# Kernel optimization log

Hardware: AMD Instinct MI355X
Metric: run time of the kernel (lower is better)

The kernel has to match this reference:

```python
import jax, jax.numpy as jnp
import numpy as np

B = 128
H = 512
S_TOK = 512
S_DESC = 128
N_NODES = 65536
MARGIN = 0.05
COS_EPS = 1e-8


def setup_inputs() -> dict:
    key = jax.random.key(0)
    ks = jax.random.split(key, 26)
    sc = 1.0 / np.sqrt(H)
    inp = {
        "token_feat": jax.random.normal(ks[0], (B, S_TOK, H), jnp.float32),
        "token_len": jnp.maximum(jax.random.randint(ks[1], (B,), 0, S_TOK), 1),
        "node_h": jax.random.normal(ks[2], (N_NODES, H), jnp.float32),
        "seg_ids": jnp.sort(jax.random.randint(ks[3], (N_NODES,), 0, B)),
        "desc_anchor_feat": jax.random.normal(ks[4], (B, S_DESC, H), jnp.float32),
        "desc_anchor_len": jnp.maximum(jax.random.randint(ks[5], (B,), 0, S_DESC), 1),
        "desc_neg_feat": jax.random.normal(ks[6], (B, S_DESC, H), jnp.float32),
        "desc_neg_len": jnp.maximum(jax.random.randint(ks[7], (B,), 0, S_DESC), 1),
        # attention params: Linear(H,H) weight/bias, Linear(H,1) weight/bias
        "Wt": jax.random.normal(ks[8], (H, H), jnp.float32) * sc,
        "bt": jax.random.normal(ks[9], (H,), jnp.float32) * sc,
        "vt": jax.random.normal(ks[10], (H,), jnp.float32) * sc,
        "ct": jax.random.normal(ks[11], (), jnp.float32) * sc,
        "Wa": jax.random.normal(ks[12], (H, H), jnp.float32) * sc,
        "ba": jax.random.normal(ks[13], (H,), jnp.float32) * sc,
        "va": jax.random.normal(ks[14], (H,), jnp.float32) * sc,
        "ca": jax.random.normal(ks[15], (), jnp.float32) * sc,
        "Wd": jax.random.normal(ks[16], (H, H), jnp.float32) * sc,
        "bd": jax.random.normal(ks[17], (H,), jnp.float32) * sc,
        "vd": jax.random.normal(ks[18], (H,), jnp.float32) * sc,
        "cd": jax.random.normal(ks[19], (), jnp.float32) * sc,
        "Wf": jax.random.normal(ks[20], (2 * H, H), jnp.float32) * sc,
        "bf": jax.random.normal(ks[21], (H,), jnp.float32) * sc,
    }
    return inp


def masked_attn_pool(feat, lens, W, b, v, c):
    # feat: [B,S,H]; lens: [B]. Masked softmax attention pooling == the
    # per-sample masked_select + softmax + bmm loop, vectorized.
    logits = jnp.einsum("bsh,h->bs", jnp.tanh(jnp.einsum("bsh,hk->bsk", feat, W) + b), v) + c
    mask = jnp.arange(feat.shape[1])[None, :] < lens[:, None]
    logits = jnp.where(mask, logits, -jnp.inf)
    w = jax.nn.softmax(logits, axis=1)  # [B,S]
    return jnp.einsum("bs,bsh->bh", w, feat)


def segment_attn_pool(h, seg, W, b, v, c, num_segments):
    # h: [N,H] packed node states; seg: [N] sample id. Per-segment softmax attn
    # pooling == the per-sample slice + softmax + bmm loop over tree_node_num.
    logits = jnp.tanh(h @ W + b) @ v + c  # [N]
    m = jax.ops.segment_max(logits, seg, num_segments=num_segments)
    e = jnp.exp(logits - m[seg])
    denom = jax.ops.segment_sum(e, seg, num_segments=num_segments)
    w = e / denom[seg]
    return jax.ops.segment_sum(w[:, None] * h, seg, num_segments=num_segments)


def cosine_sim(a, b):
    na = jnp.maximum(jnp.linalg.norm(a, axis=1), COS_EPS)
    nb = jnp.maximum(jnp.linalg.norm(b, axis=1), COS_EPS)
    return jnp.sum(a * b, axis=1) / (na * nb)


def reference(token_feat, token_len, node_h, seg_ids, desc_anchor_feat,
              desc_anchor_len, desc_neg_feat, desc_neg_len,
              Wt, bt, vt, ct, Wa, ba, va, ca, Wd, bd, vd, cd, Wf, bf):
    # token modality (use_token_attn, then use_tanh)
    tok = jnp.tanh(masked_attn_pool(token_feat, token_len, Wt, bt, vt, ct))
    # AST modality: use_tanh applies to node states BEFORE attention
    hn = jnp.tanh(node_h)
    ast = jnp.tanh(segment_attn_pool(hn, seg_ids, Wa, ba, va, ca, B))
    code_feat = jnp.tanh(jnp.concatenate([tok, ast], axis=1) @ Wf + bf)
    # desc modality: attn pool, use_tanh, then the extra unconditional tanh
    da = jnp.tanh(jnp.tanh(masked_attn_pool(desc_anchor_feat, desc_anchor_len, Wd, bd, vd, cd)))
    dn = jnp.tanh(jnp.tanh(masked_attn_pool(desc_neg_feat, desc_neg_len, Wd, bd, vd, cd)))
    anchor_sim = cosine_sim(code_feat, da)
    neg_sim = cosine_sim(code_feat, dn)
    loss = jnp.mean(jnp.maximum(MARGIN - anchor_sim + neg_sim, 1e-6))
    return loss
```

## Files before the change

kernel.cpp:

```cpp
#include <hip/hip_runtime.h>
#include <math.h>

#define HDIM 512
#define BATCH 128

typedef _Float16 f16x8 __attribute__((ext_vector_type(8)));
typedef float f32x4 __attribute__((ext_vector_type(4)));

__device__ __forceinline__ float fast_tanh(float x) {
  float e = __expf(2.0f * x);
  return 1.0f - 2.0f / (e + 1.0f);
}

__device__ __forceinline__ void gload_lds16(const void* g, void* l) {
  __builtin_amdgcn_global_load_lds(
      (const __attribute__((address_space(1))) unsigned int*)g,
      (__attribute__((address_space(3))) unsigned int*)l, 16, 0, 0);
}

template <bool TANH>
__global__ __launch_bounds__(256) void cvt_tile_kernel(
    const float* __restrict__ A, _Float16* __restrict__ A2,
    int Mtot, int m_off, int Mrows) {
  const int total = Mrows * 64;
  for (int i = blockIdx.x * 256 + threadIdx.x; i < total; i += gridDim.x * 256) {
    const int m = i >> 6, c = i & 63;
    const int kt = c >> 3, cc = c & 7;
    const float* src = A + (size_t)m * HDIM + c * 8;
    const float4 x = ((const float4*)src)[0];
    const float4 y = ((const float4*)src)[1];
    f16x8 h;
    if (TANH) {
      h[0] = (_Float16)fast_tanh(x.x); h[1] = (_Float16)fast_tanh(x.y);
      h[2] = (_Float16)fast_tanh(x.z); h[3] = (_Float16)fast_tanh(x.w);
      h[4] = (_Float16)fast_tanh(y.x); h[5] = (_Float16)fast_tanh(y.y);
      h[6] = (_Float16)fast_tanh(y.z); h[7] = (_Float16)fast_tanh(y.w);
    } else {
      h[0] = (_Float16)x.x; h[1] = (_Float16)x.y;
      h[2] = (_Float16)x.z; h[3] = (_Float16)x.w;
      h[4] = (_Float16)y.x; h[5] = (_Float16)y.y;
      h[6] = (_Float16)y.z; h[7] = (_Float16)y.w;
    }
    const int dr = m_off + m;
    char* dst = (char*)A2 + ((size_t)kt * Mtot + dr) * 128 + ((cc * 16) ^ ((dr & 7) << 4));
    *(f16x8*)dst = h;
  }
}

__global__ __launch_bounds__(256) void cvt_w3_kernel(
    const float* __restrict__ Wt, const float* __restrict__ Wa,
    const float* __restrict__ Wd, _Float16* __restrict__ W2t,
    _Float16* __restrict__ W2a, _Float16* __restrict__ W2d) {
  const int i = blockIdx.x * 256 + threadIdx.x;
  if (i >= 512 * 64) return;
  const float* W = (blockIdx.y == 0) ? Wt : (blockIdx.y == 1) ? Wa : Wd;
  _Float16* W2 = (blockIdx.y == 0) ? W2t : (blockIdx.y == 1) ? W2a : W2d;
  const int n = i & 511, g = i >> 9;
  const int kt = g >> 3, cc = g & 7;
  f16x8 h;
#pragma unroll
  for (int j = 0; j < 8; ++j)
    h[j] = (_Float16)W[(size_t)(kt * 64 + cc * 8 + j) * HDIM + n];
  char* dst = (char*)W2 + ((size_t)kt * 512 + n) * 128 + ((cc * 16) ^ ((n & 7) << 4));
  *(f16x8*)dst = h;
}

__global__ __launch_bounds__(512) void gemm_logits_pipe_kernel(
    const _Float16* __restrict__ A2, const _Float16* __restrict__ W2,
    const float* __restrict__ bias, const float* __restrict__ vvec,
    float* __restrict__ logits, int M) {
  __shared__ __align__(16) _Float16 As[2][128 * 64];
  __shared__ __align__(16) _Float16 Bs[2][128 * 64];

  const int tid = threadIdx.x;
  const int nwg = gridDim.x;
  const int qq = nwg >> 3;
  const int raw = blockIdx.x;
  const int swz = (raw & 7) * qq + (raw >> 3);
  const int nb = swz & 3;
  const int mb = swz >> 2;
  const size_t m0 = (size_t)mb * 128;
  const int n0 = nb * 128;

  const int lane = tid & 63, wid = tid >> 6;
  const int tx = lane & 15, qd = lane >> 4;
  const int wm = wid >> 1;
  const int wn = wid & 1;

  const char* gA = (const char*)A2 + m0 * 128;
  const char* gB = (const char*)W2 + (size_t)n0 * 128;
  const size_t sA = (size_t)M * 128;
  const size_t sB = (size_t)512 * 128;
  const int lo = tid * 16;
  const int wlo = wid * 1024;

  f32x4 acc[2][4];
#pragma unroll
  for (int i = 0; i < 2; ++i)
#pragma unroll
    for (int j = 0; j < 4; ++j) acc[i][j] = (f32x4){0.f, 0.f, 0.f, 0.f};

  auto STAGE = [&](int buf, int kt) {
    const char* a = gA + (size_t)kt * sA;
    const char* b = gB + (size_t)kt * sB;
#pragma unroll
    for (int p = 0; p < 2; ++p) {
      gload_lds16(a + lo + p * 8192, (char*)As[buf] + wlo + p * 8192);
      gload_lds16(b + lo + p * 8192, (char*)Bs[buf] + wlo + p * 8192);
    }
  };

  auto COMPUTE = [&](int buf) {
#pragma unroll
    for (int ks = 0; ks < 2; ++ks) {
      f16x8 aF[2], bF[4];
#pragma unroll
      for (int f = 0; f < 2; ++f) {
        const int row = wm * 32 + f * 16 + tx;
        int by = row * 128 + (ks * 32 + qd * 8) * 2;
        by ^= (row & 7) << 4;
        aF[f] = *(const f16x8*)((const char*)As[buf] + by);
      }
#pragma unroll
      for (int f = 0; f < 4; ++f) {
        const int n = wn * 64 + f * 16 + tx;
        int by = n * 128 + (ks * 32 + qd * 8) * 2;
        by ^= (n & 7) << 4;
        bF[f] = *(const f16x8*)((const char*)Bs[buf] + by);
      }
#pragma unroll
      for (int i = 0; i < 2; ++i)
#pragma unroll
        for (int j = 0; j < 4; ++j)
          acc[i][j] = __builtin_amdgcn_mfma_f32_16x16x32_f16(aF[i], bF[j], acc[i][j], 0, 0, 0);
    }
  };

  STAGE(0, 0);
#pragma unroll
  for (int t = 0; t < 8; ++t) {
    const int cur = t & 1;
    if (t < 7) {
      STAGE(cur ^ 1, t + 1);
      asm volatile("s_waitcnt vmcnt(4)" ::: "memory");
    } else {
      asm volatile("s_waitcnt vmcnt(0)" ::: "memory");
    }
    asm volatile("" ::: "memory");
    __builtin_amdgcn_s_barrier();
    asm volatile("" ::: "memory");
    __builtin_amdgcn_s_setprio(1);
    COMPUTE(cur);
    __builtin_amdgcn_s_setprio(0);
    asm volatile("" ::: "memory");
    __builtin_amdgcn_s_barrier();
    asm volatile("" ::: "memory");
  }

  float vv[4], bb[4];
#pragma unroll
  for (int j = 0; j < 4; ++j) {
    const int n = n0 + wn * 64 + j * 16 + tx;
    vv[j] = vvec[n];
    bb[j] = bias[n];
  }
#pragma unroll
  for (int i = 0; i < 2; ++i) {
#pragma unroll
    for (int r = 0; r < 4; ++r) {
      float s = 0.0f;
#pragma unroll
      for (int j = 0; j < 4; ++j)
        s = fmaf(vv[j], fast_tanh(acc[i][j][r] + bb[j]), s);
      s += __shfl_xor(s, 1);
      s += __shfl_xor(s, 2);
      s += __shfl_xor(s, 4);
      s += __shfl_xor(s, 8);
      if (tx == 0)
        atomicAdd(&logits[m0 + wm * 32 + i * 16 + qd * 4 + r], s);
    }
  }
}


__global__ void zero_kernel(float* __restrict__ p, int n) {
  const int i = blockIdx.x * 256 + threadIdx.x;
  if (i < n) p[i] = 0.0f;
}

__global__ void seg_bounds_kernel(const int* __restrict__ seg, int N,
                                  int* __restrict__ seg_start) {
  const int b = threadIdx.x;
  if (b > BATCH) return;
  int lo = 0, hi = N;
  while (lo < hi) {
    const int mid = (lo + hi) >> 1;
    if (seg[mid] < b) lo = mid + 1; else hi = mid;
  }
  seg_start[b] = lo;
}

__global__ __launch_bounds__(256) void softmax_all_kernel(
    float* __restrict__ ltok, float* __restrict__ ldesc,
    float* __restrict__ lnode, const int* __restrict__ tlen,
    const int* __restrict__ dalen, const int* __restrict__ dnlen,
    const int* __restrict__ seg_start) {
  __shared__ float smax[4], ssum[4];
  const int b = blockIdx.x, mode = blockIdx.y, tid = threadIdx.x;
  float* l;
  int s0, s1, fill_end;
  if (mode == 0)      { l = ltok + (size_t)b * 512;          s0 = 0; s1 = tlen[b];  fill_end = 512; }
  else if (mode == 1) { l = ldesc + (size_t)b * 128;         s0 = 0; s1 = dalen[b]; fill_end = 128; }
  else if (mode == 2) { l = ldesc + 16384 + (size_t)b * 128; s0 = 0; s1 = dnlen[b]; fill_end = 128; }
  else                { l = lnode; s0 = seg_start[b]; s1 = seg_start[b + 1]; fill_end = -1; }

  float mymax = -1e30f;
  for (int s = s0 + tid; s < s1; s += 256) mymax = fmaxf(mymax, l[s]);
#pragma unroll
  for (int off = 32; off; off >>= 1) mymax = fmaxf(mymax, __shfl_xor(mymax, off));
  if ((tid & 63) == 0) smax[tid >> 6] = mymax;
  __syncthreads();
  const float bmax = fmaxf(fmaxf(smax[0], smax[1]), fmaxf(smax[2], smax[3]));
  float mysum = 0.0f;
  for (int s = s0 + tid; s < s1; s += 256) mysum += __expf(l[s] - bmax);
#pragma unroll
  for (int off = 32; off; off >>= 1) mysum += __shfl_xor(mysum, off);
  if ((tid & 63) == 0) ssum[tid >> 6] = mysum;
  __syncthreads();
  const float inv = 1.0f / (ssum[0] + ssum[1] + ssum[2] + ssum[3]);
  for (int s = s0 + tid; s < s1; s += 256) l[s] = __expf(l[s] - bmax) * inv;
  if (fill_end > 0)
    for (int s = s1 + tid; s < fill_end; s += 256) l[s] = 0.0f;
}

__global__ __launch_bounds__(256) void pool_masked_all_kernel(
    const _Float16* __restrict__ A2tok, const _Float16* __restrict__ A2desc,
    const float* __restrict__ ltok, const float* __restrict__ ldesc,
    float* __restrict__ tok_pool, float* __restrict__ da_pool,
    float* __restrict__ dn_pool) {
  const int b = blockIdx.x, c = blockIdx.y, tid = threadIdx.x;
  const _Float16* A2;
  const float* w;
  float* out;
  int Mtot, rbase, s0;
  if (c < 8)       { A2 = A2tok;  Mtot = 65536; rbase = b * 512;         w = ltok;  out = tok_pool; s0 = c * 64; }
  else if (c < 10) { A2 = A2desc; Mtot = 32768; rbase = b * 128;         w = ldesc; out = da_pool;  s0 = (c - 8) * 64; }
  else             { A2 = A2desc; Mtot = 32768; rbase = 16384 + b * 128; w = ldesc; out = dn_pool;  s0 = (c - 10) * 64; }
  const int h = tid * 2;
  const int kt = h >> 6, col = h & 63;
  const char* base = (const char*)A2 + (size_t)kt * Mtot * 128;
  float ax = 0.0f, ay = 0.0f;
  for (int s = s0; s < s0 + 64; ++s) {
    const int row = rbase + s;
    const float wsc = w[row];
    if (wsc != 0.0f) {
      const unsigned u = *(const unsigned*)(base + (size_t)row * 128 + ((col * 2) ^ ((row & 7) << 4)));
      const _Float16* hp = (const _Float16*)&u;
      ax = fmaf(wsc, (float)hp[0], ax);
      ay = fmaf(wsc, (float)hp[1], ay);
    }
  }
  atomicAdd(&out[b * HDIM + h], ax);
  atomicAdd(&out[b * HDIM + h + 1], ay);
}

__global__ __launch_bounds__(256) void pool_tiled_seg_kernel(
    const _Float16* __restrict__ A2, const float* __restrict__ w,
    const int* __restrict__ seg_start, float* __restrict__ pool, int Mtot) {
  const int b = blockIdx.x, c = blockIdx.y, tid = threadIdx.x;
  const int h = tid * 2;
  const int kt = h >> 6, col = h & 63;
  const char* base = (const char*)A2 + (size_t)kt * Mtot * 128;
  const int s0 = seg_start[b], s1 = seg_start[b + 1];
  const int nseg = s1 - s0;
  const int chunk = (nseg + (int)gridDim.y - 1) / (int)gridDim.y;
  const int a0 = s0 + c * chunk;
  const int a1 = min(s1, a0 + chunk);
  float ax = 0.0f, ay = 0.0f;
  for (int s = a0; s < a1; ++s) {
    const float wsc = w[s];
    const unsigned u = *(const unsigned*)(base + (size_t)s * 128 + ((col * 2) ^ ((s & 7) << 4)));
    const _Float16* hp = (const _Float16*)&u;
    ax = fmaf(wsc, (float)hp[0], ax);
    ay = fmaf(wsc, (float)hp[1], ay);
  }
  atomicAdd(&pool[b * HDIM + h], ax);
  atomicAdd(&pool[b * HDIM + h + 1], ay);
}

__global__ __launch_bounds__(256) void code_gemm_kernel(
    const float* __restrict__ tok_pool, const float* __restrict__ ast_pool,
    const float* __restrict__ Wf, float* __restrict__ parts) {
  __shared__ float catS[128][65];
  __shared__ float4 wfS[64][32];
  const int nb = blockIdx.x, kb = blockIdx.y, tid = threadIdx.x;
  const int k0 = kb * 64;
  const float* src = (k0 < 512) ? (tok_pool + k0) : (ast_pool + (k0 - 512));
  for (int i = tid; i < 128 * 16; i += 256) {
    const int r = i >> 4, c4 = i & 15;
    const float4 v = *(const float4*)(src + (size_t)r * HDIM + c4 * 4);
    catS[r][c4 * 4 + 0] = fast_tanh(v.x);
    catS[r][c4 * 4 + 1] = fast_tanh(v.y);
    catS[r][c4 * 4 + 2] = fast_tanh(v.z);
    catS[r][c4 * 4 + 3] = fast_tanh(v.w);
  }
  for (int i = tid; i < 64 * 32; i += 256) {
    const int r = i >> 5, c = i & 31;
    wfS[r][c] = *(const float4*)(Wf + (size_t)(k0 + r) * HDIM + nb * 128 + c * 4);
  }
  __syncthreads();
  const int tb = tid >> 4, tn = tid & 15;
  const int b0 = tb * 8, n0l = tn * 8;
  float acc[8][8];
#pragma unroll
  for (int i = 0; i < 8; ++i)
#pragma unroll
    for (int j = 0; j < 8; ++j) acc[i][j] = 0.0f;
  for (int k = 0; k < 64; ++k) {
    float a[8];
#pragma unroll
    for (int i = 0; i < 8; ++i) a[i] = catS[b0 + i][k];
    const float4 w0 = wfS[k][tn * 2], w1 = wfS[k][tn * 2 + 1];
    const float wv[8] = {w0.x, w0.y, w0.z, w0.w, w1.x, w1.y, w1.z, w1.w};
#pragma unroll
    for (int i = 0; i < 8; ++i)
#pragma unroll
      for (int j = 0; j < 8; ++j) acc[i][j] = fmaf(a[i], wv[j], acc[i][j]);
  }
  float* dst = parts + ((size_t)kb * 128) * HDIM + nb * 128;
#pragma unroll
  for (int i = 0; i < 8; ++i) {
    const float4 o0 = {acc[i][0], acc[i][1], acc[i][2], acc[i][3]};
    const float4 o1 = {acc[i][4], acc[i][5], acc[i][6], acc[i][7]};
    *(float4*)(dst + (size_t)(b0 + i) * HDIM + n0l) = o0;
    *(float4*)(dst + (size_t)(b0 + i) * HDIM + n0l + 4) = o1;
  }
}

__global__ __launch_bounds__(256) void sims_kernel(
    const float* __restrict__ parts, const float* __restrict__ bfv,
    const float* __restrict__ da_pool, const float* __restrict__ dn_pool,
    float* __restrict__ terms) {
  __shared__ float sr[4][5];
  const int b = blockIdx.x, tid = threadIdx.x;
  float c2 = 0, a2 = 0, n2 = 0, ca = 0, cn = 0;
  for (int i = tid; i < HDIM; i += 256) {
    float pre = bfv[i];
#pragma unroll
    for (int kb = 0; kb < 16; ++kb)
      pre += parts[((size_t)kb * 128 + b) * HDIM + i];
    const float cf = fast_tanh(pre);
    const float av = fast_tanh(fast_tanh(da_pool[(size_t)b * HDIM + i]));
    const float nv = fast_tanh(fast_tanh(dn_pool[(size_t)b * HDIM + i]));
    c2 = fmaf(cf, cf, c2); a2 = fmaf(av, av, a2); n2 = fmaf(nv, nv, n2);
    ca = fmaf(cf, av, ca); cn = fmaf(cf, nv, cn);
  }
#pragma unroll
  for (int off = 32; off; off >>= 1) {
    c2 += __shfl_xor(c2, off); a2 += __shfl_xor(a2, off); n2 += __shfl_xor(n2, off);
    ca += __shfl_xor(ca, off); cn += __shfl_xor(cn, off);
  }
  const int wv = tid >> 6;
  if ((tid & 63) == 0) {
    sr[wv][0] = c2; sr[wv][1] = a2; sr[wv][2] = n2; sr[wv][3] = ca; sr[wv][4] = cn;
  }
  __syncthreads();
  if (tid == 0) {
    c2 = sr[0][0] + sr[1][0] + sr[2][0] + sr[3][0];
    a2 = sr[0][1] + sr[1][1] + sr[2][1] + sr[3][1];
    n2 = sr[0][2] + sr[1][2] + sr[2][2] + sr[3][2];
    ca = sr[0][3] + sr[1][3] + sr[2][3] + sr[3][3];
    cn = sr[0][4] + sr[1][4] + sr[2][4] + sr[3][4];
    const float nc = fmaxf(sqrtf(c2), 1e-8f);
    const float na = fmaxf(sqrtf(a2), 1e-8f);
    const float nn = fmaxf(sqrtf(n2), 1e-8f);
    terms[b] = fmaxf(0.05f - ca / (nc * na) + cn / (nc * nn), 1e-6f);
  }
}

__global__ void loss_kernel(const float* __restrict__ terms, float* __restrict__ out) {
  const int tid = threadIdx.x;
  float v = terms[tid];
#pragma unroll
  for (int off = 32; off; off >>= 1) v += __shfl_xor(v, off);
  __shared__ float sr[2];
  if ((tid & 63) == 0) sr[tid >> 6] = v;
  __syncthreads();
  if (tid == 0) out[0] = (sr[0] + sr[1]) * (1.0f / (float)BATCH);
}


extern "C" void kernel_launch(void* const* d_in, const int* in_sizes, int n_in,
                              void* d_out, int out_size, void* d_ws, size_t ws_size,
                              hipStream_t stream) {
  (void)in_sizes; (void)n_in; (void)out_size; (void)ws_size;
  const float* token_feat = (const float*)d_in[0];
  const int*   token_len  = (const int*)d_in[1];
  const float* node_h     = (const float*)d_in[2];
  const int*   seg_ids    = (const int*)d_in[3];
  const float* da_feat    = (const float*)d_in[4];
  const int*   da_len     = (const int*)d_in[5];
  const float* dn_feat    = (const float*)d_in[6];
  const int*   dn_len     = (const int*)d_in[7];
  const float* Wt = (const float*)d_in[8];
  const float* bt = (const float*)d_in[9];
  const float* vt = (const float*)d_in[10];
  const float* Wa = (const float*)d_in[12];
  const float* ba = (const float*)d_in[13];
  const float* va = (const float*)d_in[14];
  const float* Wd = (const float*)d_in[16];
  const float* bd = (const float*)d_in[17];
  const float* vd = (const float*)d_in[18];
  const float* Wf  = (const float*)d_in[20];
  const float* bfv = (const float*)d_in[21];

  const int MTOK = 65536;
  const int MDESC2 = 32768;
  const int NNODES = 65536;

  float* ws = (float*)d_ws;
  float* logits_tok  = ws;
  float* logits_node = logits_tok + MTOK;
  float* logits_desc = logits_node + NNODES;
  float* tok_pool    = logits_desc + MDESC2;
  float* ast_pool    = tok_pool + 128 * HDIM;
  float* da_pool     = ast_pool + 128 * HDIM;
  float* dn_pool     = da_pool + 128 * HDIM;
  float* terms       = dn_pool + 128 * HDIM;
  int*   seg_start   = (int*)(terms + 128);
  float* parts       = (float*)(seg_start + 256);
  _Float16* W2t = (_Float16*)(parts + 16 * 128 * HDIM);
  _Float16* W2a = W2t + HDIM * HDIM;
  _Float16* W2d = W2a + HDIM * HDIM;
  _Float16* A2tok  = W2d + HDIM * HDIM;
  _Float16* A2node = A2tok + (size_t)8 * MTOK * 64;
  _Float16* A2desc = A2node + (size_t)8 * NNODES * 64;

  const int ZTOT = MTOK + NNODES + MDESC2 + 4 * 128 * HDIM;
  zero_kernel<<<dim3((ZTOT + 255) / 256), 256, 0, stream>>>(ws, ZTOT);
  seg_bounds_kernel<<<1, 256, 0, stream>>>(seg_ids, NNODES, seg_start);

  cvt_w3_kernel<<<dim3(128, 3), 256, 0, stream>>>(Wt, Wa, Wd, W2t, W2a, W2d);
  cvt_tile_kernel<false><<<2048, 256, 0, stream>>>(token_feat, A2tok, MTOK, 0, MTOK);
  cvt_tile_kernel<true ><<<2048, 256, 0, stream>>>(node_h, A2node, NNODES, 0, NNODES);
  cvt_tile_kernel<false><<<1024, 256, 0, stream>>>(da_feat, A2desc, MDESC2, 0, 16384);
  cvt_tile_kernel<false><<<1024, 256, 0, stream>>>(dn_feat, A2desc, MDESC2, 16384, 16384);

  gemm_logits_pipe_kernel<<<MTOK / 128 * 4, 512, 0, stream>>>(A2tok, W2t, bt, vt, logits_tok, MTOK);
  gemm_logits_pipe_kernel<<<NNODES / 128 * 4, 512, 0, stream>>>(A2node, W2a, ba, va, logits_node, NNODES);
  gemm_logits_pipe_kernel<<<MDESC2 / 128 * 4, 512, 0, stream>>>(A2desc, W2d, bd, vd, logits_desc, MDESC2);

  softmax_all_kernel<<<dim3(BATCH, 4), 256, 0, stream>>>(
      logits_tok, logits_desc, logits_node, token_len, da_len, dn_len, seg_start);

  pool_masked_all_kernel<<<dim3(BATCH, 12), 256, 0, stream>>>(
      A2tok, A2desc, logits_tok, logits_desc, tok_pool, da_pool, dn_pool);
  pool_tiled_seg_kernel<<<dim3(BATCH, 4), 256, 0, stream>>>(
      A2node, logits_node, seg_start, ast_pool, NNODES);

  code_gemm_kernel<<<dim3(4, 16), 256, 0, stream>>>(tok_pool, ast_pool, Wf, parts);
  sims_kernel<<<BATCH, 256, 0, stream>>>(parts, bfv, da_pool, dn_pool, terms);
  loss_kernel<<<1, 128, 0, stream>>>(terms, (float*)d_out);
}
```

Baseline: 374.4 us.

## Enlarge logits GEMM tile to 256x256 and split B staging mid-iteration

The fused GEMM+tanh+dot logits kernel now uses 256x256 output tiles per 512-thread block instead of 128x128, with each wave computing a 128x64 sub-tile (8x4 MFMA accumulators). This raises arithmetic intensity per LDS and global load and halves the number of atomic partial-logit writes per row across N-blocks. The K-step is split into two halves so the next B tile is staged between them, overlapping loads with MFMA work. In exchange, LDS use rises to 128 KB per block and register pressure grows (128 accumulator floats), which may limit occupancy despite the launch-bounds hint and leave fewer blocks to fill the device.

```diff
diff --git a/kernel.cpp b/kernel.cpp
--- a/kernel.cpp
+++ b/kernel.cpp
@@ -65,27 +65,27 @@
   *(f16x8*)dst = h;
 }
 
-__global__ __launch_bounds__(512) void gemm_logits_pipe_kernel(
+__global__ __launch_bounds__(512, 2) void gemm_logits_p2_kernel(
     const _Float16* __restrict__ A2, const _Float16* __restrict__ W2,
     const float* __restrict__ bias, const float* __restrict__ vvec,
     float* __restrict__ logits, int M) {
-  __shared__ __align__(16) _Float16 As[2][128 * 64];
-  __shared__ __align__(16) _Float16 Bs[2][128 * 64];
+  __shared__ __align__(16) _Float16 As[2][256 * 64];
+  __shared__ __align__(16) _Float16 Bs[2][256 * 64];
 
   const int tid = threadIdx.x;
   const int nwg = gridDim.x;
   const int qq = nwg >> 3;
   const int raw = blockIdx.x;
   const int swz = (raw & 7) * qq + (raw >> 3);
-  const int nb = swz & 3;
-  const int mb = swz >> 2;
-  const size_t m0 = (size_t)mb * 128;
-  const int n0 = nb * 128;
+  const int nb = swz & 1;
+  const int mb = swz >> 1;
+  const size_t m0 = (size_t)mb * 256;
+  const int n0 = nb * 256;
 
   const int lane = tid & 63, wid = tid >> 6;
   const int tx = lane & 15, qd = lane >> 4;
-  const int wm = wid >> 1;
-  const int wn = wid & 1;
+  const int wm = wid >> 2;
+  const int wn = wid & 3;
 
   const char* gA = (const char*)A2 + m0 * 128;
   const char* gB = (const char*)W2 + (size_t)n0 * 128;
@@ -94,64 +94,69 @@
   const int lo = tid * 16;
   const int wlo = wid * 1024;
 
-  f32x4 acc[2][4];
-#pragma unroll
-  for (int i = 0; i < 2; ++i)
+  f32x4 acc[8][4];
+#pragma unroll
+  for (int i = 0; i < 8; ++i)
 #pragma unroll
     for (int j = 0; j < 4; ++j) acc[i][j] = (f32x4){0.f, 0.f, 0.f, 0.f};
 
-  auto STAGE = [&](int buf, int kt) {
+  auto STAGE_A = [&](int buf, int kt) {
     const char* a = gA + (size_t)kt * sA;
+#pragma unroll
+    for (int p = 0; p < 4; ++p)
+      gload_lds16(a + lo + p * 8192, (char*)As[buf] + wlo + p * 8192);
+  };
+  auto STAGE_B = [&](int buf, int kt) {
     const char* b = gB + (size_t)kt * sB;
 #pragma unroll
-    for (int p = 0; p < 2; ++p) {
-      gload_lds16(a + lo + p * 8192, (char*)As[buf] + wlo + p * 8192);
+    for (int p = 0; p < 4; ++p)
       gload_lds16(b + lo + p * 8192, (char*)Bs[buf] + wlo + p * 8192);
-    }
   };
 
-  auto COMPUTE = [&](int buf) {
-#pragma unroll
-    for (int ks = 0; ks < 2; ++ks) {
-      f16x8 aF[2], bF[4];
-#pragma unroll
-      for (int f = 0; f < 2; ++f) {
-        const int row = wm * 32 + f * 16 + tx;
-        int by = row * 128 + (ks * 32 + qd * 8) * 2;
-        by ^= (row & 7) << 4;
-        aF[f] = *(const f16x8*)((const char*)As[buf] + by);
-      }
-#pragma unroll
-      for (int f = 0; f < 4; ++f) {
-        const int n = wn * 64 + f * 16 + tx;
-        int by = n * 128 + (ks * 32 + qd * 8) * 2;
-        by ^= (n & 7) << 4;
-        bF[f] = *(const f16x8*)((const char*)Bs[buf] + by);
-      }
-#pragma unroll
-      for (int i = 0; i < 2; ++i)
-#pragma unroll
-        for (int j = 0; j < 4; ++j)
-          acc[i][j] = __builtin_amdgcn_mfma_f32_16x16x32_f16(aF[i], bF[j], acc[i][j], 0, 0, 0);
-    }
+  auto HALF = [&](int buf, int ks) {
+    f16x8 aF[8], bF[4];
+#pragma unroll
+    for (int i = 0; i < 8; ++i) {
+      const int row = wm * 128 + i * 16 + tx;
+      int by = row * 128 + (ks * 32 + qd * 8) * 2;
+      by ^= (row & 7) << 4;
+      aF[i] = *(const f16x8*)((const char*)As[buf] + by);
+    }
+#pragma unroll
+    for (int j = 0; j < 4; ++j) {
+      const int n = wn * 64 + j * 16 + tx;
+      int by = n * 128 + (ks * 32 + qd * 8) * 2;
+      by ^= (n & 7) << 4;
+      bF[j] = *(const f16x8*)((const char*)Bs[buf] + by);
+    }
+    __builtin_amdgcn_s_setprio(1);
+#pragma unroll
+    for (int i = 0; i < 8; ++i)
+#pragma unroll
+      for (int j = 0; j < 4; ++j)
+        acc[i][j] = __builtin_amdgcn_mfma_f32_16x16x32_f16(aF[i], bF[j], acc[i][j], 0, 0, 0);
+    __builtin_amdgcn_s_setprio(0);
   };
 
-  STAGE(0, 0);
+  STAGE_A(0, 0);
+  STAGE_B(0, 0);
 #pragma unroll
   for (int t = 0; t < 8; ++t) {
     const int cur = t & 1;
     if (t < 7) {
-      STAGE(cur ^ 1, t + 1);
+      STAGE_A(cur ^ 1, t + 1);
       asm volatile("s_waitcnt vmcnt(4)" ::: "memory");
     } else {
       asm volatile("s_waitcnt vmcnt(0)" ::: "memory");
     }
+    __builtin_amdgcn_s_barrier();
+    asm volatile("" ::: "memory");
+    HALF(cur, 0);
     asm volatile("" ::: "memory");
     __builtin_amdgcn_s_barrier();
     asm volatile("" ::: "memory");
-    __builtin_amdgcn_s_setprio(1);
-    COMPUTE(cur);
-    __builtin_amdgcn_s_setprio(0);
+    if (t < 7) STAGE_B(cur ^ 1, t + 1);
+    HALF(cur, 1);
     asm volatile("" ::: "memory");
     __builtin_amdgcn_s_barrier();
     asm volatile("" ::: "memory");
@@ -165,7 +170,7 @@
     bb[j] = bias[n];
   }
 #pragma unroll
-  for (int i = 0; i < 2; ++i) {
+  for (int i = 0; i < 8; ++i) {
 #pragma unroll
     for (int r = 0; r < 4; ++r) {
       float s = 0.0f;
@@ -177,7 +182,7 @@
       s += __shfl_xor(s, 4);
       s += __shfl_xor(s, 8);
       if (tx == 0)
-        atomicAdd(&logits[m0 + wm * 32 + i * 16 + qd * 4 + r], s);
+        atomicAdd(&logits[m0 + wm * 128 + i * 16 + qd * 4 + r], s);
     }
   }
 }
@@ -446,9 +451,9 @@
   cvt_tile_kernel<false><<<1024, 256, 0, stream>>>(da_feat, A2desc, MDESC2, 0, 16384);
   cvt_tile_kernel<false><<<1024, 256, 0, stream>>>(dn_feat, A2desc, MDESC2, 16384, 16384);
 
-  gemm_logits_pipe_kernel<<<MTOK / 128 * 4, 512, 0, stream>>>(A2tok, W2t, bt, vt, logits_tok, MTOK);
-  gemm_logits_pipe_kernel<<<NNODES / 128 * 4, 512, 0, stream>>>(A2node, W2a, ba, va, logits_node, NNODES);
-  gemm_logits_pipe_kernel<<<MDESC2 / 128 * 4, 512, 0, stream>>>(A2desc, W2d, bd, vd, logits_desc, MDESC2);
+  gemm_logits_p2_kernel<<<MTOK / 256 * 2, 512, 0, stream>>>(A2tok, W2t, bt, vt, logits_tok, MTOK);
+  gemm_logits_p2_kernel<<<NNODES / 256 * 2, 512, 0, stream>>>(A2node, W2a, ba, va, logits_node, NNODES);
+  gemm_logits_p2_kernel<<<MDESC2 / 256 * 2, 512, 0, stream>>>(A2desc, W2d, bd, vd, logits_desc, MDESC2);
 
   softmax_all_kernel<<<dim3(BATCH, 4), 256, 0, stream>>>(
       logits_tok, logits_desc, logits_node, token_len, da_len, dn_len, seg_start);
```

Result: faster. 352.9 us (-5.7%).
